# Kernel tuning notes

Hardware: AMD Instinct MI355X
Metric: run time of the kernel (lower is better)

Reference implementation:

```python
import jax, jax.numpy as jnp
import numpy as np
from jax import lax

B, DF, DO, DK, DV, KER, STR = 32, 2048, 2048, 128, 128, 4, 2
STR_Q = int(np.ceil(DF / DO))  # = 1, so query conv has kernel=stride=1


def conv1d(x, w, stride):
    # x: [B, Cin, L], w: [Cout, Cin, K] -> [B, Cout, Lout], VALID, no bias
    return lax.conv_general_dilated(x, w, (stride,), 'VALID',
                                    dimension_numbers=('NCH', 'OIH', 'NCH'))


def layernorm(x, w, b, eps):
    m = jnp.mean(x, axis=-1, keepdims=True)
    v = jnp.mean(jnp.square(x - m), axis=-1, keepdims=True)
    return (x - m) * lax.rsqrt(v + eps) * w + b


def setup_inputs() -> dict:
    key = jax.random.key(0)
    ks = jax.random.split(key, 10)
    s = 0.02
    return {
        'features': jax.random.normal(ks[0], (B, DF), dtype=jnp.float32),
        'shuffled_index': jax.random.randint(ks[1], (DF,), 0, DF, dtype=jnp.int32),
        'ln_w': jnp.ones((DF,), jnp.float32),
        'ln_b': jnp.zeros((DF,), jnp.float32),
        'q_w': jax.random.normal(ks[2], (DK, 1, STR_Q), jnp.float32) * s,
        'k_w': jax.random.normal(ks[3], (DK, 1, KER), jnp.float32) * s,
        'v_w': jax.random.normal(ks[4], (DV, 1, KER), jnp.float32) * s,
        'conv_w': jax.random.normal(ks[5], (1, DV, 1), jnp.float32) * s,
        'bn_ln_w': jnp.ones((DO,), jnp.float32),
        'bn_ln_b': jnp.zeros((DO,), jnp.float32),
        'w1_w': jax.random.normal(ks[6], (DO, DO), jnp.float32) * s,
        'w1_b': jnp.zeros((DO,), jnp.float32),
        'w2_w': jax.random.normal(ks[7], (DO, DO), jnp.float32) * s,
        'w2_b': jnp.zeros((DO,), jnp.float32),
    }


def reference(features, shuffled_index, ln_w, ln_b, q_w, k_w, v_w, conv_w,
              bn_ln_w, bn_ln_b, w1_w, w1_b, w2_w, w2_b):
    residual = features                               # [B, DF]
    q_in = layernorm(features, ln_w, ln_b, 1e-5)[:, None, :]   # [B,1,DF]
    shuf = features[:, shuffled_index][:, None, :]             # [B,1,DF]

    query = conv1d(q_in, q_w, STR_Q)                  # [B, DK, DO]
    key_t = conv1d(shuf, k_w, STR)                    # [B, DK, NC]
    value = conv1d(shuf, v_w, STR)                    # [B, DV, NC]

    # ScaledDotProduction, temperature=1, dropout eval-mode identity
    attn = jnp.einsum('bkq,bkc->bqc', query, key_t)   # [B, DO, NC]
    attn = jax.nn.softmax(attn, axis=2)
    out = jnp.einsum('bqc,bvc->bqv', attn, value)     # [B, DO, DV]

    # output Conv1d(d_v -> 1, kernel 1) applied to [B, DV, DO]
    out = jnp.einsum('bqv,v->bq', out, conv_w[0, :, 0])  # [B, DO]
    out = out + residual                              # d_features == d_out

    # Bottleneck FFN
    r = out
    h = layernorm(out, bn_ln_w, bn_ln_b, 1e-6)
    h = jax.nn.relu(h @ w1_w.T + w1_b) @ w2_w.T + w2_b
    out = h + r
    return (out, attn)
```

## Files before the change

### kernel.cpp

```cpp
#include <hip/hip_runtime.h>
#include <float.h>

#define NB 32
#define D  2048
#define NC 1023
#define RPB 8

typedef float f32x4 __attribute__((ext_vector_type(4)));

#define OFF_LN   0
#define OFF_SW   (NB*D)
#define OFF_MM   (OFF_SW + 2*NB*NC)
#define OFF_OUT1 (OFF_MM + 2*NB)
#define OFF_LN2  (OFF_OUT1 + NB*D)
#define OFF_H    (OFF_LN2 + NB*D)

__device__ __forceinline__ float wred_sum(float x){
  #pragma unroll
  for (int o = 32; o; o >>= 1) x += __shfl_xor(x, o);
  return x;
}

__global__ __launch_bounds__(256) void prep_kernel(
    const float* __restrict__ feat, const int* __restrict__ idx,
    const float* __restrict__ ln_w, const float* __restrict__ ln_b,
    const float* __restrict__ q_w,  const float* __restrict__ k_w,
    const float* __restrict__ v_w,  const float* __restrict__ conv_w,
    float* __restrict__ ws)
{
  __shared__ float sh_feat[D];
  __shared__ float sh_shuf[D];
  __shared__ float red_s[4][2];
  __shared__ float red_k[4][8];
  __shared__ float red_mm[4][2];

  const int b = blockIdx.x;
  const int t = threadIdx.x;
  const int wid = t >> 6;

  const float4* fb4 = (const float4*)(feat + b * D);
  float4* sf4 = (float4*)sh_feat;
  float4 fv[2];
  float s1 = 0.f, s2 = 0.f;
  #pragma unroll
  for (int j = 0; j < 2; ++j) {
    float4 v = fb4[t + j * 256];
    fv[j] = v;
    sf4[t + j * 256] = v;
    s1 += (v.x + v.y) + (v.z + v.w);
    s2 += fmaf(v.x, v.x, fmaf(v.y, v.y, fmaf(v.z, v.z, v.w * v.w)));
  }

  float pk[4] = {0,0,0,0}, pv[4] = {0,0,0,0};
  if (t < 128) {
    float qv = q_w[t], cv = conv_w[t];
    #pragma unroll
    for (int j = 0; j < 4; ++j) {
      pk[j] = qv * k_w[t * 4 + j];
      pv[j] = cv * v_w[t * 4 + j];
    }
  }
  s1 = wred_sum(s1); s2 = wred_sum(s2);
  #pragma unroll
  for (int j = 0; j < 4; ++j) { pk[j] = wred_sum(pk[j]); pv[j] = wred_sum(pv[j]); }
  if ((t & 63) == 0) {
    red_s[wid][0] = s1; red_s[wid][1] = s2;
    #pragma unroll
    for (int j = 0; j < 4; ++j) { red_k[wid][j] = pk[j]; red_k[wid][4 + j] = pv[j]; }
  }
  __syncthreads();

  const float S1 = red_s[0][0] + red_s[1][0] + red_s[2][0] + red_s[3][0];
  const float S2 = red_s[0][1] + red_s[1][1] + red_s[2][1] + red_s[3][1];
  float kq[4], vw[4];
  #pragma unroll
  for (int j = 0; j < 4; ++j) {
    kq[j] = red_k[0][j] + red_k[1][j] + red_k[2][j] + red_k[3][j];
    vw[j] = red_k[0][4+j] + red_k[1][4+j] + red_k[2][4+j] + red_k[3][4+j];
  }
  const float mean = S1 * (1.f / D);
  const float rstd = rsqrtf(S2 * (1.f / D) - mean * mean + 1e-5f);

  float* lnp = ws + OFF_LN + b * D;
  const float4* lw4 = (const float4*)ln_w;
  const float4* lb4 = (const float4*)ln_b;
  #pragma unroll
  for (int j = 0; j < 2; ++j) {
    int i = t + j * 256;
    float4 v = fv[j], w = lw4[i], bb = lb4[i], o;
    o.x = (v.x - mean) * rstd * w.x + bb.x;
    o.y = (v.y - mean) * rstd * w.y + bb.y;
    o.z = (v.z - mean) * rstd * w.z + bb.z;
    o.w = (v.w - mean) * rstd * w.w + bb.w;
    ((float4*)lnp)[i] = o;
  }

  #pragma unroll
  for (int j = 0; j < 8; ++j) {
    int i = t + j * 256;
    sh_shuf[i] = sh_feat[idx[i]];
  }
  __syncthreads();

  float2* swp = (float2*)(ws + OFF_SW) + b * NC;
  float lmax = -FLT_MAX, lmin = FLT_MAX;
  #pragma unroll
  for (int j = 0; j < 4; ++j) {
    int c = t + j * 256;
    if (c < NC) {
      float a0 = sh_shuf[2*c], a1 = sh_shuf[2*c+1], a2 = sh_shuf[2*c+2], a3 = sh_shuf[2*c+3];
      float sv = fmaf(a0, kq[0], fmaf(a1, kq[1], fmaf(a2, kq[2], a3 * kq[3])));
      float wv = fmaf(a0, vw[0], fmaf(a1, vw[1], fmaf(a2, vw[2], a3 * vw[3])));
      float2 p; p.x = sv; p.y = wv;
      swp[c] = p;
      lmax = fmaxf(lmax, sv);
      lmin = fminf(lmin, sv);
    }
  }
  #pragma unroll
  for (int o = 32; o; o >>= 1) {
    lmax = fmaxf(lmax, __shfl_xor(lmax, o));
    lmin = fminf(lmin, __shfl_xor(lmin, o));
  }
  if ((t & 63) == 0) { red_mm[wid][0] = lmax; red_mm[wid][1] = lmin; }
  __syncthreads();
  if (t == 0) {
    ws[OFF_MM + b]      = fmaxf(fmaxf(red_mm[0][0], red_mm[1][0]), fmaxf(red_mm[2][0], red_mm[3][0]));
    ws[OFF_MM + NB + b] = fminf(fminf(red_mm[0][1], red_mm[1][1]), fminf(red_mm[2][1], red_mm[3][1]));
  }
}

__global__ __launch_bounds__(256) void attn_kernel(
    const float* __restrict__ feat, float* __restrict__ ws,
    float* __restrict__ out)
{
  __shared__ float ebuf[RPB * 1024];
  __shared__ float sinv[RPB];

  const int row0 = blockIdx.x * RPB;
  const int b = row0 >> 11;
  const int t = threadIdx.x;
  const int wid = t >> 6, lane = t & 63;

  const float smax = ws[OFF_MM + b], smin = ws[OFF_MM + NB + b];
  const float2* sw = (const float2*)(ws + OFF_SW) + b * NC;

  #pragma unroll
  for (int rr = 0; rr < 2; ++rr) {
    const int r = wid * 2 + rr;
    const int row = row0 + r;
    const float alpha = ws[OFF_LN + row];
    const float m = (alpha >= 0.f) ? alpha * smax : alpha * smin;
    float* eb = ebuf + r * NC;
    float l = 0.f, acc = 0.f;
    #pragma unroll
    for (int j = 0; j < 16; ++j) {
      int c = lane + j * 64;
      if (c < NC) {
        float2 p = sw[c];
        float e = __expf(fmaf(alpha, p.x, -m));
        eb[c] = e;
        l += e;
        acc = fmaf(e, p.y, acc);
      }
    }
    #pragma unroll
    for (int o = 32; o; o >>= 1) { l += __shfl_xor(l, o); acc += __shfl_xor(acc, o); }
    if (lane == 0) {
      float inv = 1.f / l;
      sinv[r] = inv;
      ws[OFF_OUT1 + row] = fmaf(acc, inv, feat[row]);
    }
  }
  __syncthreads();

  f32x4* base = (f32x4*)(out + NB * D + (size_t)row0 * NC);
  const f32x4* eb4 = (const f32x4*)ebuf;
  #pragma unroll
  for (int j = 0; j < 8; ++j) {
    int i4 = t + j * 256;
    if (i4 < 2046) {
      f32x4 v = eb4[i4];
      int g = i4 * 4;
      int r0 = g / NC, r1 = (g + 1) / NC, r2 = (g + 2) / NC, r3 = (g + 3) / NC;
      v.x *= sinv[r0]; v.y *= sinv[r1]; v.z *= sinv[r2]; v.w *= sinv[r3];
      __builtin_nontemporal_store(v, base + i4);
    }
  }
}

__global__ __launch_bounds__(256) void ln2_init_kernel(
    const float* __restrict__ bnw, const float* __restrict__ bnb,
    const float* __restrict__ w1b, const float* __restrict__ w2b,
    float* __restrict__ ws, float* __restrict__ out)
{
  __shared__ float red_s[4][2];
  const int b = blockIdx.x, t = threadIdx.x;
  const int wid = t >> 6;
  const float4* x4 = (const float4*)(ws + OFF_OUT1 + b * D);
  float4 xv[2];
  float s1 = 0.f, s2 = 0.f;
  #pragma unroll
  for (int j = 0; j < 2; ++j) {
    float4 v = x4[t + j * 256];
    xv[j] = v;
    s1 += (v.x + v.y) + (v.z + v.w);
    s2 += fmaf(v.x, v.x, fmaf(v.y, v.y, fmaf(v.z, v.z, v.w * v.w)));
  }
  s1 = wred_sum(s1); s2 = wred_sum(s2);
  if ((t & 63) == 0) { red_s[wid][0] = s1; red_s[wid][1] = s2; }
  __syncthreads();
  const float S1 = red_s[0][0] + red_s[1][0] + red_s[2][0] + red_s[3][0];
  const float S2 = red_s[0][1] + red_s[1][1] + red_s[2][1] + red_s[3][1];
  const float mean = S1 * (1.f / D);
  const float rstd = rsqrtf(S2 * (1.f / D) - mean * mean + 1e-6f);

  float4* ln2p = (float4*)(ws + OFF_LN2 + b * D);
  float4* hp   = (float4*)(ws + OFF_H   + b * D);
  float4* op   = (float4*)out + b * (D / 4);
  const float4* bw4 = (const float4*)bnw;
  const float4* bb4 = (const float4*)bnb;
  const float4* w1b4 = (const float4*)w1b;
  const float4* w2b4 = (const float4*)w2b;
  #pragma unroll
  for (int j = 0; j < 2; ++j) {
    int i = t + j * 256;
    float4 v = xv[j], w = bw4[i], bb = bb4[i], o;
    o.x = (v.x - mean) * rstd * w.x + bb.x;
    o.y = (v.y - mean) * rstd * w.y + bb.y;
    o.z = (v.z - mean) * rstd * w.z + bb.z;
    o.w = (v.w - mean) * rstd * w.w + bb.w;
    ln2p[i] = o;
    hp[i] = w1b4[i];
    float4 w2 = w2b4[i], oo;
    oo.x = v.x + w2.x; oo.y = v.y + w2.y; oo.z = v.z + w2.z; oo.w = v.w + w2.w;
    op[i] = oo;
  }
}

template<int RELU>
__global__ __launch_bounds__(256) void gemm_kernel(
    const float* __restrict__ X, const float* __restrict__ W,
    float* __restrict__ out)
{
  __shared__ float xs[32 * 68];
  __shared__ float wt[32 * 68];
  const int nb = blockIdx.x & 63;
  const int kb = blockIdx.x >> 6;
  const int n0 = nb * 32;
  const int t = threadIdx.x;
  const int row = t >> 3, kl = t & 7;
  const int tr = t >> 4, tc = (t & 15) * 4;

  float acc[32];
  #pragma unroll
  for (int m = 0; m < 32; ++m) acc[m] = 0.f;

  for (int ch = 0; ch < 4; ++ch) {
    const int kc = kb * 256 + ch * 64;
    #pragma unroll
    for (int jj = 0; jj < 2; ++jj) {
      int r = tr + jj * 16;
      float4 v = *(const float4*)(X + r * 2048 + kc + tc);
      if (RELU) {
        v.x = fmaxf(v.x, 0.f); v.y = fmaxf(v.y, 0.f);
        v.z = fmaxf(v.z, 0.f); v.w = fmaxf(v.w, 0.f);
      }
      *(float4*)(xs + r * 68 + tc) = v;
      float4 wv = *(const float4*)(W + (n0 + r) * 2048 + kc + tc);
      *(float4*)(wt + r * 68 + tc) = wv;
    }
    __syncthreads();
    const float4 wa = *(float4*)(wt + row * 68 + kl * 8);
    const float4 wb = *(float4*)(wt + row * 68 + kl * 8 + 4);
    #pragma unroll
    for (int m = 0; m < 32; ++m) {
      float4 xa = *(float4*)(xs + m * 68 + kl * 8);
      float4 xb = *(float4*)(xs + m * 68 + kl * 8 + 4);
      acc[m] = fmaf(xa.x, wa.x, fmaf(xa.y, wa.y, fmaf(xa.z, wa.z, fmaf(xa.w, wa.w,
               fmaf(xb.x, wb.x, fmaf(xb.y, wb.y, fmaf(xb.z, wb.z, fmaf(xb.w, wb.w, acc[m]))))))));
    }
    __syncthreads();
  }
  #pragma unroll
  for (int m = 0; m < 32; ++m) {
    acc[m] += __shfl_xor(acc[m], 1);
    acc[m] += __shfl_xor(acc[m], 2);
    acc[m] += __shfl_xor(acc[m], 4);
  }
  #pragma unroll
  for (int i = 0; i < 4; ++i) {
    int m = kl * 4 + i;
    atomicAdd(out + m * 2048 + n0 + row, acc[m]);
  }
}

extern "C" void kernel_launch(void* const* d_in, const int* in_sizes, int n_in,
                              void* d_out, int out_size, void* d_ws, size_t ws_size,
                              hipStream_t stream)
{
  (void)in_sizes; (void)n_in; (void)out_size; (void)ws_size;
  const float* feat   = (const float*)d_in[0];
  const int*   idx    = (const int*)d_in[1];
  const float* ln_w   = (const float*)d_in[2];
  const float* ln_b   = (const float*)d_in[3];
  const float* q_w    = (const float*)d_in[4];
  const float* k_w    = (const float*)d_in[5];
  const float* v_w    = (const float*)d_in[6];
  const float* conv_w = (const float*)d_in[7];
  const float* bnw    = (const float*)d_in[8];
  const float* bnb    = (const float*)d_in[9];
  const float* w1w    = (const float*)d_in[10];
  const float* w1b    = (const float*)d_in[11];
  const float* w2w    = (const float*)d_in[12];
  const float* w2b    = (const float*)d_in[13];
  float* out = (float*)d_out;
  float* ws  = (float*)d_ws;

  prep_kernel<<<dim3(NB), dim3(256), 0, stream>>>(feat, idx, ln_w, ln_b, q_w, k_w, v_w, conv_w, ws);
  attn_kernel<<<dim3(NB * D / RPB), dim3(256), 0, stream>>>(feat, ws, out);
  ln2_init_kernel<<<dim3(NB), dim3(256), 0, stream>>>(bnw, bnb, w1b, w2b, ws, out);
  gemm_kernel<0><<<dim3(512), dim3(256), 0, stream>>>(ws + OFF_LN2, w1w, ws + OFF_H);
  gemm_kernel<1><<<dim3(512), dim3(256), 0, stream>>>(ws + OFF_H, w2w, out);
}
```

Measured before the change: 354.3 us.

## Stage score table in LDS and retile split-K FFN GEMM with register blocking

The attention kernel now copies the per-batch score/value pairs into shared memory once per block, instead of having each wave read them from global memory. The FFN GEMM is restructured to a 32x64 output tile over a 128-wide K slice with 128 threads. Each thread computes a 4x4 register block from an XOR-swizzled transposed weight tile, which lowers LDS reads per FMA and removes the shuffle reduction. It adds an extra barrier in the attention kernel and more atomics per thread in the GEMM.

```diff
diff --git a/kernel.cpp b/kernel.cpp
--- a/kernel.cpp
+++ b/kernel.cpp
@@ -11,7 +11,7 @@
 #define OFF_LN   0
 #define OFF_SW   (NB*D)
 #define OFF_MM   (OFF_SW + 2*NB*NC)
-#define OFF_OUT1 (OFF_MM + 2*NB)
+#define OFF_OUT1 (OFF_MM + 64)
 #define OFF_LN2  (OFF_OUT1 + NB*D)
 #define OFF_H    (OFF_LN2 + NB*D)
 
@@ -135,6 +135,7 @@
     float* __restrict__ out)
 {
   __shared__ float ebuf[RPB * 1024];
+  __shared__ float2 sws[1024];
   __shared__ float sinv[RPB];
 
   const int row0 = blockIdx.x * RPB;
@@ -143,7 +144,13 @@
   const int wid = t >> 6, lane = t & 63;
 
   const float smax = ws[OFF_MM + b], smin = ws[OFF_MM + NB + b];
-  const float2* sw = (const float2*)(ws + OFF_SW) + b * NC;
+  const float2* swg = (const float2*)(ws + OFF_SW) + b * NC;
+  #pragma unroll
+  for (int j = 0; j < 4; ++j) {
+    int c = t + j * 256;
+    if (c < NC) sws[c] = swg[c];
+  }
+  __syncthreads();
 
   #pragma unroll
   for (int rr = 0; rr < 2; ++rr) {
@@ -157,7 +164,7 @@
     for (int j = 0; j < 16; ++j) {
       int c = lane + j * 64;
       if (c < NC) {
-        float2 p = sw[c];
+        float2 p = sws[c];
         float e = __expf(fmaf(alpha, p.x, -m));
         eb[c] = e;
         l += e;
@@ -239,60 +246,79 @@
 }
 
 template<int RELU>
-__global__ __launch_bounds__(256) void gemm_kernel(
+__global__ __launch_bounds__(128) void gemm_kernel(
     const float* __restrict__ X, const float* __restrict__ W,
     float* __restrict__ out)
 {
-  __shared__ float xs[32 * 68];
-  __shared__ float wt[32 * 68];
-  const int nb = blockIdx.x & 63;
-  const int kb = blockIdx.x >> 6;
-  const int n0 = nb * 32;
+  __shared__ float xs[32][132];
+  __shared__ float wtT[128 * 64];
+  const int nb = blockIdx.x & 31;
+  const int kb = blockIdx.x >> 5;
+  const int n0 = nb * 64;
+  const int k0 = kb * 128;
   const int t = threadIdx.x;
-  const int row = t >> 3, kl = t & 7;
-  const int tr = t >> 4, tc = (t & 15) * 4;
-
-  float acc[32];
-  #pragma unroll
-  for (int m = 0; m < 32; ++m) acc[m] = 0.f;
-
-  for (int ch = 0; ch < 4; ++ch) {
-    const int kc = kb * 256 + ch * 64;
-    #pragma unroll
-    for (int jj = 0; jj < 2; ++jj) {
-      int r = tr + jj * 16;
-      float4 v = *(const float4*)(X + r * 2048 + kc + tc);
-      if (RELU) {
-        v.x = fmaxf(v.x, 0.f); v.y = fmaxf(v.y, 0.f);
-        v.z = fmaxf(v.z, 0.f); v.w = fmaxf(v.w, 0.f);
-      }
-      *(float4*)(xs + r * 68 + tc) = v;
-      float4 wv = *(const float4*)(W + (n0 + r) * 2048 + kc + tc);
-      *(float4*)(wt + r * 68 + tc) = wv;
-    }
-    __syncthreads();
-    const float4 wa = *(float4*)(wt + row * 68 + kl * 8);
-    const float4 wb = *(float4*)(wt + row * 68 + kl * 8 + 4);
-    #pragma unroll
-    for (int m = 0; m < 32; ++m) {
-      float4 xa = *(float4*)(xs + m * 68 + kl * 8);
-      float4 xb = *(float4*)(xs + m * 68 + kl * 8 + 4);
-      acc[m] = fmaf(xa.x, wa.x, fmaf(xa.y, wa.y, fmaf(xa.z, wa.z, fmaf(xa.w, wa.w,
-               fmaf(xb.x, wb.x, fmaf(xb.y, wb.y, fmaf(xb.z, wb.z, fmaf(xb.w, wb.w, acc[m]))))))));
-    }
-    __syncthreads();
-  }
-  #pragma unroll
-  for (int m = 0; m < 32; ++m) {
-    acc[m] += __shfl_xor(acc[m], 1);
-    acc[m] += __shfl_xor(acc[m], 2);
-    acc[m] += __shfl_xor(acc[m], 4);
-  }
-  #pragma unroll
-  for (int i = 0; i < 4; ++i) {
-    int m = kl * 4 + i;
-    atomicAdd(out + m * 2048 + n0 + row, acc[m]);
-  }
+  const int tm = t >> 4;
+  const int tn = t & 15;
+
+  #pragma unroll
+  for (int jj = 0; jj < 8; ++jj) {
+    int idx = jj * 128 + t;
+    int m_r = idx >> 5, q_r = idx & 31;
+    float4 v = *(const float4*)(X + m_r * 2048 + k0 + q_r * 4);
+    if (RELU) {
+      v.x = fmaxf(v.x, 0.f); v.y = fmaxf(v.y, 0.f);
+      v.z = fmaxf(v.z, 0.f); v.w = fmaxf(v.w, 0.f);
+    }
+    *(float4*)(&xs[m_r][q_r * 4]) = v;
+  }
+  #pragma unroll
+  for (int jj = 0; jj < 16; ++jj) {
+    int idx = jj * 128 + t;
+    int n_r = idx >> 5, q_r = idx & 31;
+    float4 v = *(const float4*)(W + (n0 + n_r) * 2048 + k0 + q_r * 4);
+    float vv[4] = {v.x, v.y, v.z, v.w};
+    #pragma unroll
+    for (int c = 0; c < 4; ++c) {
+      int kk = q_r * 4 + c;
+      wtT[kk * 64 + ((((n_r >> 2) ^ (kk & 15)) << 2) | (n_r & 3))] = vv[c];
+    }
+  }
+  __syncthreads();
+
+  float4 acc0 = {0,0,0,0}, acc1 = {0,0,0,0}, acc2 = {0,0,0,0}, acc3 = {0,0,0,0};
+  #pragma unroll 2
+  for (int kq = 0; kq < 32; ++kq) {
+    float4 xq0 = *(const float4*)(&xs[tm * 4 + 0][kq * 4]);
+    float4 xq1 = *(const float4*)(&xs[tm * 4 + 1][kq * 4]);
+    float4 xq2 = *(const float4*)(&xs[tm * 4 + 2][kq * 4]);
+    float4 xq3 = *(const float4*)(&xs[tm * 4 + 3][kq * 4]);
+    #pragma unroll
+    for (int c = 0; c < 4; ++c) {
+      int kk = kq * 4 + c;
+      float4 wv = *(const float4*)(&wtT[kk * 64 + ((tn ^ (kk & 15)) << 2)]);
+      float x0 = (c==0)?xq0.x:(c==1)?xq0.y:(c==2)?xq0.z:xq0.w;
+      float x1 = (c==0)?xq1.x:(c==1)?xq1.y:(c==2)?xq1.z:xq1.w;
+      float x2 = (c==0)?xq2.x:(c==1)?xq2.y:(c==2)?xq2.z:xq2.w;
+      float x3 = (c==0)?xq3.x:(c==1)?xq3.y:(c==2)?xq3.z:xq3.w;
+      acc0.x = fmaf(x0, wv.x, acc0.x); acc0.y = fmaf(x0, wv.y, acc0.y);
+      acc0.z = fmaf(x0, wv.z, acc0.z); acc0.w = fmaf(x0, wv.w, acc0.w);
+      acc1.x = fmaf(x1, wv.x, acc1.x); acc1.y = fmaf(x1, wv.y, acc1.y);
+      acc1.z = fmaf(x1, wv.z, acc1.z); acc1.w = fmaf(x1, wv.w, acc1.w);
+      acc2.x = fmaf(x2, wv.x, acc2.x); acc2.y = fmaf(x2, wv.y, acc2.y);
+      acc2.z = fmaf(x2, wv.z, acc2.z); acc2.w = fmaf(x2, wv.w, acc2.w);
+      acc3.x = fmaf(x3, wv.x, acc3.x); acc3.y = fmaf(x3, wv.y, acc3.y);
+      acc3.z = fmaf(x3, wv.z, acc3.z); acc3.w = fmaf(x3, wv.w, acc3.w);
+    }
+  }
+
+  float* op0 = out + (tm * 4 + 0) * 2048 + n0 + tn * 4;
+  float* op1 = op0 + 2048;
+  float* op2 = op1 + 2048;
+  float* op3 = op2 + 2048;
+  atomicAdd(op0+0, acc0.x); atomicAdd(op0+1, acc0.y); atomicAdd(op0+2, acc0.z); atomicAdd(op0+3, acc0.w);
+  atomicAdd(op1+0, acc1.x); atomicAdd(op1+1, acc1.y); atomicAdd(op1+2, acc1.z); atomicAdd(op1+3, acc1.w);
+  atomicAdd(op2+0, acc2.x); atomicAdd(op2+1, acc2.y); atomicAdd(op2+2, acc2.z); atomicAdd(op2+3, acc2.w);
+  atomicAdd(op3+0, acc3.x); atomicAdd(op3+1, acc3.y); atomicAdd(op3+2, acc3.z); atomicAdd(op3+3, acc3.w);
 }
 
 extern "C" void kernel_launch(void* const* d_in, const int* in_sizes, int n_in,
@@ -320,6 +346,6 @@
   prep_kernel<<<dim3(NB), dim3(256), 0, stream>>>(feat, idx, ln_w, ln_b, q_w, k_w, v_w, conv_w, ws);
   attn_kernel<<<dim3(NB * D / RPB), dim3(256), 0, stream>>>(feat, ws, out);
   ln2_init_kernel<<<dim3(NB), dim3(256), 0, stream>>>(bnw, bnb, w1b, w2b, ws, out);
-  gemm_kernel<0><<<dim3(512), dim3(256), 0, stream>>>(ws + OFF_LN2, w1w, ws + OFF_H);
-  gemm_kernel<1><<<dim3(512), dim3(256), 0, stream>>>(ws + OFF_H, w2w, out);
-}
+  gemm_kernel<0><<<dim3(512), dim3(128), 0, stream>>>(ws + OFF_LN2, w1w, ws + OFF_H);
+  gemm_kernel<1><<<dim3(512), dim3(128), 0, stream>>>(ws + OFF_H, w2w, out);
+}
```

New measurement: 374.8 us. 5.8% more time.
